# Optimization experiments

Hardware: AMD Instinct MI355X
Metric: run time of the kernel (lower is better)

Reference implementation:

```python
import jax, jax.numpy as jnp
import numpy as np

B, S, E, H, NQ, FF = 2, 2048, 768, 12, 8, 3072
DK = E // H
EPS = 1e-5


def _layernorm(x, g, b):
    m = jnp.mean(x, axis=-1, keepdims=True)
    v = jnp.mean((x - m) ** 2, axis=-1, keepdims=True)
    return (x - m) * jax.lax.rsqrt(v + EPS) * g + b


def setup_inputs() -> dict:
    key = jax.random.key(0)
    ks = jax.random.split(key, 12)
    s = 0.02
    return {
        'x': jax.random.normal(ks[0], (B, S, E), dtype=jnp.float32),
        'W_o': jax.random.normal(ks[1], (E, E), dtype=jnp.float32) * s,
        'b_o': jnp.zeros((E,), dtype=jnp.float32),
        'g1': jnp.ones((E,), dtype=jnp.float32),
        'be1': jnp.zeros((E,), dtype=jnp.float32),
        'g2': jnp.ones((E,), dtype=jnp.float32),
        'be2': jnp.zeros((E,), dtype=jnp.float32),
        'ry': jax.random.normal(ks[2], (NQ,), dtype=jnp.float32),
        'W1': jax.random.normal(ks[3], (NQ, FF), dtype=jnp.float32) * s,
        'b1': jnp.zeros((FF,), dtype=jnp.float32),
        'W2': jax.random.normal(ks[4], (FF, E), dtype=jnp.float32) * s,
        'b2': jnp.zeros((E,), dtype=jnp.float32),
    }


def reference(x, W_o, b_o, g1, be1, g2, be2, ry, W1, b1, W2, b2):
    # --- multi-head self-attention (q = k = v = x, no QKV projection) ---
    q = x.reshape(B, S, H, DK).transpose(0, 2, 1, 3)  # [B,H,S,DK]
    scores = jnp.einsum('bhqd,bhkd->bhqk', q, q) / jnp.sqrt(jnp.float32(DK))
    attn = jax.nn.softmax(scores, axis=-1)
    out = jnp.einsum('bhqk,bhkd->bhqd', attn, q)
    out = out.transpose(0, 2, 1, 3).reshape(B, S, E)
    attn_out = out @ W_o + b_o

    x = _layernorm(x + attn_out, g1, be1)

    # --- quantum FFN: per-wire RX(x_i) encode, RY(ry_i), <Z> = cos(x_i)*cos(ry_i) ---
    q_meas = jnp.cos(x[..., :NQ]) * jnp.cos(ry)  # [B,S,NQ]
    ffn_out = jax.nn.relu(q_meas @ W1 + b1) @ W2 + b2

    return _layernorm(x + ffn_out, g2, be2)
```

## Files before the change

kernel.cpp:

```cpp
#include <hip/hip_runtime.h>
#include <hip/hip_bf16.h>

#define B_  2
#define S_  2048
#define E_  768
#define H_  12
#define DK_ 64
#define NQ_ 8
#define FF_ 3072
#define EPS_ 1e-5f

typedef __attribute__((ext_vector_type(8))) short short8;
typedef __attribute__((ext_vector_type(4))) float f32x4;
typedef __hip_bfloat16 bf16;

__device__ __forceinline__ bf16 f2bh(float f) { return __float2bfloat16(f); }
__device__ __forceinline__ short f2b(float f) {
    bf16 h = __float2bfloat16(f);
    return *reinterpret_cast<short*>(&h);
}

__device__ __forceinline__ int swz(int row, int col) {
    return (col & 7) | ((((col >> 3) ^ (row & 7)) & 7) << 3);
}

__device__ __forceinline__ f32x4 mfma16(short8 a, short8 b, f32x4 c) {
    return __builtin_amdgcn_mfma_f32_16x16x32_bf16(a, b, c, 0, 0, 0);
}

__global__ __launch_bounds__(256) void prep_cvt(const float* __restrict__ x,
                                                bf16* __restrict__ xb, int n4) {
    int i = blockIdx.x * 256 + threadIdx.x;
    if (i >= n4) return;
    float4 f = *(const float4*)(x + (size_t)i * 4);
    short4 sv;
    sv.x = f2b(f.x); sv.y = f2b(f.y); sv.z = f2b(f.z); sv.w = f2b(f.w);
    *(short4*)((short*)xb + (size_t)i * 4) = sv;
}

__global__ __launch_bounds__(256) void transpose_cvt(const float* __restrict__ W,
                                                     bf16* __restrict__ WT,
                                                     int K, int N) {
    __shared__ float tile[32][33];
    int k0 = blockIdx.y * 32, n0 = blockIdx.x * 32;
    int tx = threadIdx.x & 31, ty = threadIdx.x >> 5;
#pragma unroll
    for (int i = 0; i < 4; i++) {
        int row = ty + i * 8;
        tile[row][tx] = W[(size_t)(k0 + row) * N + n0 + tx];
    }
    __syncthreads();
#pragma unroll
    for (int i = 0; i < 4; i++) {
        int row = ty + i * 8;
        WT[(size_t)(n0 + row) * K + k0 + tx] = f2bh(tile[tx][row]);
    }
}

__global__ __launch_bounds__(256) void attn_kernel(const bf16* __restrict__ xb,
                                                   bf16* __restrict__ out) {
    const int qtiles = S_ / 64;
    const int nwg = B_ * H_ * qtiles;
    int o = blockIdx.x;
    int blk = (o & 7) * (nwg >> 3) + (o >> 3);
    int qt = blk % qtiles;
    int hh = (blk / qtiles) % H_;
    int bb = blk / (qtiles * H_);
    const bf16* base = xb + (size_t)bb * S_ * E_ + hh * DK_;

    __shared__ __align__(16) bf16 Ks[64][64];
    __shared__ __align__(16) bf16 Vt[64][64];
    __shared__ __align__(16) bf16 Pl[4][16][64];

    int t = threadIdx.x;
    int w = t >> 6, l = t & 63, c = l & 15, g = l >> 4;

    short8 qf[2];
    {
        const bf16* qp = base + (size_t)(qt * 64 + w * 16 + c) * E_;
        qf[0] = *(const short8*)(qp + g * 8);
        qf[1] = *(const short8*)(qp + 32 + g * 8);
    }

    f32x4 oacc[4];
    float l_part[4];
#pragma unroll
    for (int n = 0; n < 4; n++) { oacc[n] = (f32x4){0.f, 0.f, 0.f, 0.f}; l_part[n] = 0.f; }

    int skey = t & 63;
    int scb0 = t >> 6;

    short8 pre[2];
#pragma unroll
    for (int it = 0; it < 2; it++)
        pre[it] = *(const short8*)(base + (size_t)skey * E_ + (scb0 + it * 4) * 8);

    for (int kt = 0; kt < S_ / 64; kt++) {
#pragma unroll
        for (int it = 0; it < 2; it++) {
            int cb = scb0 + it * 4;
            *(short8*)&Ks[skey][swz(skey, cb * 8)] = pre[it];
#pragma unroll
            for (int j = 0; j < 8; j++) {
                int d = cb * 8 + j;
                short sv = pre[it][j];
                Vt[d][swz(d, skey)] = *reinterpret_cast<bf16*>(&sv);
            }
        }
        __syncthreads();

        if (kt + 1 < S_ / 64) {
#pragma unroll
            for (int it = 0; it < 2; it++)
                pre[it] = *(const short8*)(base + (size_t)((kt + 1) * 64 + skey) * E_ + (scb0 + it * 4) * 8);
        }

        f32x4 sfr[4];
#pragma unroll
        for (int n = 0; n < 4; n++) {
            sfr[n] = (f32x4){0.f, 0.f, 0.f, 0.f};
#pragma unroll
            for (int kh = 0; kh < 2; kh++) {
                const short8 bfr = *(const short8*)&Ks[n * 16 + c][swz(n * 16 + c, kh * 32 + g * 8)];
                sfr[n] = mfma16(qf[kh], bfr, sfr[n]);
            }
        }
#pragma unroll
        for (int jj = 0; jj < 4; jj++) {
            float pv[4];
#pragma unroll
            for (int n = 0; n < 4; n++)
                pv[n] = exp2f(sfr[n][jj] * 0.18033688f);
            l_part[jj] += (pv[0] + pv[1]) + (pv[2] + pv[3]);
            int r = g * 4 + jj;
#pragma unroll
            for (int n = 0; n < 4; n++)
                Pl[w][r][swz(r, n * 16 + c)] = f2bh(pv[n]);
        }

#pragma unroll
        for (int ks = 0; ks < 2; ks++) {
            short8 vb[4];
#pragma unroll
            for (int dn = 0; dn < 4; dn++)
                vb[dn] = *(const short8*)&Vt[dn * 16 + c][swz(dn * 16 + c, ks * 32 + g * 8)];
            const short8 pa = *(const short8*)&Pl[w][c][swz(c, ks * 32 + g * 8)];
#pragma unroll
            for (int dn = 0; dn < 4; dn++)
                oacc[dn] = mfma16(pa, vb[dn], oacc[dn]);
        }
        __syncthreads();
    }

#pragma unroll
    for (int jj = 0; jj < 4; jj++) {
        float lv = l_part[jj];
#pragma unroll
        for (int msk = 1; msk < 16; msk <<= 1) lv += __shfl_xor(lv, msk);
        float inv = 1.f / lv;
        size_t ro = ((size_t)bb * S_ + qt * 64 + w * 16 + g * 4 + jj) * E_ + hh * DK_;
#pragma unroll
        for (int dn = 0; dn < 4; dn++)
            out[ro + dn * 16 + c] = f2bh(oacc[dn][jj] * inv);
    }
}

__global__ __launch_bounds__(256) void gemm_bf16(const bf16* __restrict__ A,
                                                 const bf16* __restrict__ BT,
                                                 const float* __restrict__ bias,
                                                 bf16* __restrict__ C,
                                                 int M, int N, int K) {
    __shared__ __align__(16) bf16 As[64][64];
    __shared__ __align__(16) bf16 Bs[64][64];
    int nbx = gridDim.x, nwg = nbx * gridDim.y;
    int id = blockIdx.y * nbx + blockIdx.x;
    int id2 = (nwg & 7) ? id : ((id & 7) * (nwg >> 3) + (id >> 3));
    int row0 = (id2 / nbx) * 64, col0 = (id2 % nbx) * 64;
    int t = threadIdx.x, w = t >> 6, l = t & 63, c = l & 15, g = l >> 4;

    f32x4 acc[4];
#pragma unroll
    for (int n = 0; n < 4; n++) acc[n] = (f32x4){0.f, 0.f, 0.f, 0.f};

    int srow = t & 63, scb = t >> 6;
    const bf16* arow_p = A + (size_t)(row0 + srow) * K;
    const bf16* brow_p = BT + (size_t)(col0 + srow) * K;

    short8 preA[2], preB[2];
#pragma unroll
    for (int it = 0; it < 2; it++) {
        preA[it] = *(const short8*)(arow_p + (scb + it * 4) * 8);
        preB[it] = *(const short8*)(brow_p + (scb + it * 4) * 8);
    }

    for (int k0 = 0; k0 < K; k0 += 64) {
#pragma unroll
        for (int it = 0; it < 2; it++) {
            int cb = scb + it * 4;
            *(short8*)&As[srow][swz(srow, cb * 8)] = preA[it];
            *(short8*)&Bs[srow][swz(srow, cb * 8)] = preB[it];
        }
        __syncthreads();
        if (k0 + 64 < K) {
#pragma unroll
            for (int it = 0; it < 2; it++) {
                preA[it] = *(const short8*)(arow_p + k0 + 64 + (scb + it * 4) * 8);
                preB[it] = *(const short8*)(brow_p + k0 + 64 + (scb + it * 4) * 8);
            }
        }
#pragma unroll
        for (int kh = 0; kh < 2; kh++) {
            const short8 af = *(const short8*)&As[w * 16 + c][swz(w * 16 + c, kh * 32 + g * 8)];
#pragma unroll
            for (int n = 0; n < 4; n++) {
                const short8 bfr = *(const short8*)&Bs[n * 16 + c][swz(n * 16 + c, kh * 32 + g * 8)];
                acc[n] = mfma16(af, bfr, acc[n]);
            }
        }
        __syncthreads();
    }
#pragma unroll
    for (int jj = 0; jj < 4; jj++) {
        int row = row0 + w * 16 + g * 4 + jj;
#pragma unroll
        for (int n = 0; n < 4; n++) {
            int col = col0 + n * 16 + c;
            C[(size_t)row * N + col] = f2bh(acc[n][jj] + bias[col]);
        }
    }
}

__global__ __launch_bounds__(256) void gemm2_mfma(const float* __restrict__ xln,
                                                  const float* __restrict__ ry,
                                                  const float* __restrict__ W1,
                                                  const float* __restrict__ b1,
                                                  const bf16* __restrict__ W2bT,
                                                  const float* __restrict__ b2,
                                                  bf16* __restrict__ C) {
    __shared__ __align__(16) bf16 As[64][64];
    __shared__ __align__(16) bf16 Bs[64][64];
    __shared__ __align__(16) bf16 W1t[64][8];
    __shared__ __align__(16) bf16 qm_s[64][8];
    const int nbx = E_ / 64;
    const int nwg = nbx * (B_ * S_ / 64);
    int id = blockIdx.y * nbx + blockIdx.x;
    int id2 = (id & 7) * (nwg >> 3) + (id >> 3);
    int row0 = (id2 / nbx) * 64, col0 = (id2 % nbx) * 64;
    int t = threadIdx.x, w = t >> 6, l = t & 63, c = l & 15, g = l >> 4;

    if (t < 64) {
        const float* xp = xln + (size_t)(row0 + t) * E_;
#pragma unroll
        for (int i = 0; i < NQ_; i++)
            qm_s[t][i] = f2bh(cosf(xp[i]) * cosf(ry[i]));
    }

    f32x4 acc[4];
#pragma unroll
    for (int n = 0; n < 4; n++) acc[n] = (f32x4){0.f, 0.f, 0.f, 0.f};

    int srow = t & 63, scb = t >> 6;
    int cl = t & 63, ib = t >> 6;
    const bf16* brow_p = W2bT + (size_t)(col0 + srow) * FF_;

    short8 preB[2];
    float preW1[2];
    float pb1[4];
#pragma unroll
    for (int it = 0; it < 2; it++)
        preB[it] = *(const short8*)(brow_p + (scb + it * 4) * 8);
    preW1[0] = W1[(size_t)ib * FF_ + cl];
    preW1[1] = W1[(size_t)(ib + 4) * FF_ + cl];
#pragma unroll
    for (int n = 0; n < 4; n++) pb1[n] = b1[n * 16 + c];

    __syncthreads();

    for (int k0 = 0; k0 < FF_; k0 += 64) {
        float b1c[4];
#pragma unroll
        for (int n = 0; n < 4; n++) b1c[n] = pb1[n];

#pragma unroll
        for (int it = 0; it < 2; it++)
            *(short8*)&Bs[srow][swz(srow, (scb + it * 4) * 8)] = preB[it];
        W1t[cl][ib]     = f2bh(preW1[0]);
        W1t[cl][ib + 4] = f2bh(preW1[1]);
        __syncthreads();

        if (k0 + 64 < FF_) {
#pragma unroll
            for (int it = 0; it < 2; it++)
                preB[it] = *(const short8*)(brow_p + k0 + 64 + (scb + it * 4) * 8);
            preW1[0] = W1[(size_t)ib * FF_ + k0 + 64 + cl];
            preW1[1] = W1[(size_t)(ib + 4) * FF_ + k0 + 64 + cl];
#pragma unroll
            for (int n = 0; n < 4; n++) pb1[n] = b1[k0 + 64 + n * 16 + c];
        }

        short8 zz = {0, 0, 0, 0, 0, 0, 0, 0};
        short8 aq = zz;
        if (g == 0) aq = *(const short8*)&qm_s[w * 16 + c][0];
        f32x4 zero4 = {0.f, 0.f, 0.f, 0.f};
#pragma unroll
        for (int n = 0; n < 4; n++) {
            short8 bw = zz;
            if (g == 0) bw = *(const short8*)&W1t[n * 16 + c][0];
            f32x4 hfr = mfma16(aq, bw, zero4);
#pragma unroll
            for (int jj = 0; jj < 4; jj++) {
                float hv = fmaxf(hfr[jj] + b1c[n], 0.f);
                int r = w * 16 + g * 4 + jj;
                As[r][swz(r, n * 16 + c)] = f2bh(hv);
            }
        }

#pragma unroll
        for (int kh = 0; kh < 2; kh++) {
            const short8 af = *(const short8*)&As[w * 16 + c][swz(w * 16 + c, kh * 32 + g * 8)];
#pragma unroll
            for (int n = 0; n < 4; n++) {
                const short8 bfr = *(const short8*)&Bs[n * 16 + c][swz(n * 16 + c, kh * 32 + g * 8)];
                acc[n] = mfma16(af, bfr, acc[n]);
            }
        }
        __syncthreads();
    }
#pragma unroll
    for (int jj = 0; jj < 4; jj++) {
        int row = row0 + w * 16 + g * 4 + jj;
#pragma unroll
        for (int n = 0; n < 4; n++) {
            int col = col0 + n * 16 + c;
            C[(size_t)row * E_ + col] = f2bh(acc[n][jj] + b2[col]);
        }
    }
}

__global__ __launch_bounds__(256) void gemm2_fused(const float* __restrict__ xln,
                                                   const float* __restrict__ ry,
                                                   const float* __restrict__ W1,
                                                   const float* __restrict__ b1,
                                                   const float* __restrict__ W2,
                                                   const float* __restrict__ b2,
                                                   bf16* __restrict__ C) {
    __shared__ __align__(16) bf16 As[64][64];
    __shared__ __align__(16) bf16 Bst[64][64];
    __shared__ float qmS[64][NQ_];
    int row0 = blockIdx.y * 64, col0 = blockIdx.x * 64;
    int t = threadIdx.x, w = t >> 6, l = t & 63, c = l & 15, g = l >> 4;

    for (int idx = t; idx < 64 * NQ_; idx += 256) {
        int r = idx >> 3, i = idx & 7;
        qmS[r][i] = cosf(xln[(size_t)(row0 + r) * E_ + i]) * cosf(ry[i]);
    }

    f32x4 acc[4];
#pragma unroll
    for (int n = 0; n < 4; n++) acc[n] = (f32x4){0.f, 0.f, 0.f, 0.f};

    int kl = t & 63, rg = (t >> 6) * 16;
    int brow = t >> 4, bcol = (t & 15) * 4;

    for (int k0 = 0; k0 < FF_; k0 += 64) {
        __syncthreads();
        {
            float w1v[NQ_];
#pragma unroll
            for (int i = 0; i < NQ_; i++) w1v[i] = W1[i * FF_ + k0 + kl];
            float b1v = b1[k0 + kl];
#pragma unroll
            for (int r16 = 0; r16 < 16; r16++) {
                int r = rg + r16;
                float sh = b1v;
#pragma unroll
                for (int i = 0; i < NQ_; i++) sh += qmS[r][i] * w1v[i];
                As[r][swz(r, kl)] = f2bh(fmaxf(sh, 0.f));
            }
        }
#pragma unroll
        for (int it = 0; it < 4; it++) {
            int kk = brow + it * 16;
            float4 v = *(const float4*)(W2 + (size_t)(k0 + kk) * E_ + col0 + bcol);
            Bst[bcol + 0][swz(bcol + 0, kk)] = f2bh(v.x);
            Bst[bcol + 1][swz(bcol + 1, kk)] = f2bh(v.y);
            Bst[bcol + 2][swz(bcol + 2, kk)] = f2bh(v.z);
            Bst[bcol + 3][swz(bcol + 3, kk)] = f2bh(v.w);
        }
        __syncthreads();
#pragma unroll
        for (int kh = 0; kh < 2; kh++) {
            const short8 af = *(const short8*)&As[w * 16 + c][swz(w * 16 + c, kh * 32 + g * 8)];
#pragma unroll
            for (int n = 0; n < 4; n++) {
                const short8 bfr = *(const short8*)&Bst[n * 16 + c][swz(n * 16 + c, kh * 32 + g * 8)];
                acc[n] = mfma16(af, bfr, acc[n]);
            }
        }
    }
#pragma unroll
    for (int jj = 0; jj < 4; jj++) {
        int row = row0 + w * 16 + g * 4 + jj;
#pragma unroll
        for (int n = 0; n < 4; n++) {
            int col = col0 + n * 16 + c;
            C[(size_t)row * E_ + col] = f2bh(acc[n][jj] + b2[col]);
        }
    }
}

__global__ __launch_bounds__(256) void ln_add_b(const float* __restrict__ X,
                                                const bf16* __restrict__ Yb,
                                                const float* __restrict__ g,
                                                const float* __restrict__ be,
                                                float* __restrict__ out) {
    int r = blockIdx.x;
    const size_t off = (size_t)r * E_;
    int t = threadIdx.x;
    float v[3];
    float s = 0.f, s2 = 0.f;
#pragma unroll
    for (int j = 0; j < 3; j++) {
        int e = t + j * 256;
        float val = X[off + e] + __bfloat162float(Yb[off + e]);
        v[j] = val; s += val; s2 += val * val;
    }
#pragma unroll
    for (int msk = 32; msk > 0; msk >>= 1) {
        s += __shfl_xor(s, msk);
        s2 += __shfl_xor(s2, msk);
    }
    __shared__ float red[8];
    int lane = t & 63, wv = t >> 6;
    if (lane == 0) { red[wv] = s; red[4 + wv] = s2; }
    __syncthreads();
    if (t == 0) {
        red[0] = red[0] + red[1] + red[2] + red[3];
        red[4] = red[4] + red[5] + red[6] + red[7];
    }
    __syncthreads();
    float mean = red[0] * (1.f / E_);
    float var = red[4] * (1.f / E_) - mean * mean;
    float inv = rsqrtf(var + EPS_);
#pragma unroll
    for (int j = 0; j < 3; j++) {
        int e = t + j * 256;
        out[off + e] = (v[j] - mean) * inv * g[e] + be[e];
    }
}

extern "C" void kernel_launch(void* const* d_in, const int* in_sizes, int n_in,
                              void* d_out, int out_size, void* d_ws, size_t ws_size,
                              hipStream_t stream) {
    const float* x   = (const float*)d_in[0];
    const float* W_o = (const float*)d_in[1];
    const float* b_o = (const float*)d_in[2];
    const float* g1  = (const float*)d_in[3];
    const float* be1 = (const float*)d_in[4];
    const float* g2  = (const float*)d_in[5];
    const float* be2 = (const float*)d_in[6];
    const float* ry  = (const float*)d_in[7];
    const float* W1  = (const float*)d_in[8];
    const float* b1  = (const float*)d_in[9];
    const float* W2  = (const float*)d_in[10];
    const float* b2  = (const float*)d_in[11];
    float* out = (float*)d_out;

    const size_t BSE = (size_t)B_ * S_ * E_;
    char* ws = (char*)d_ws;

    const size_t FAST_NEED = 37355520;
    bool fast = ws_size >= FAST_NEED;

    bf16* xb    = (bf16*)(ws + 0);
    bf16* attnb = (bf16*)(ws + 6291456);
    bf16* WobT  = fast ? (bf16*)(ws + 12582912) : (bf16*)(ws + 18874368);
    bf16* W2bT  = (bf16*)(ws + 13762560);
    bf16* tmp1b = fast ? (bf16*)(ws + 18481152) : (bf16*)(ws + 12582912);
    float* xln  = (float*)(ws + (fast ? 24772608 : 20054016));
    bf16* tmp2b = tmp1b;

    prep_cvt<<<dim3((BSE / 4 + 255) / 256), 256, 0, stream>>>(x, xb, BSE / 4);
    transpose_cvt<<<dim3(E_ / 32, E_ / 32), 256, 0, stream>>>(W_o, WobT, E_, E_);
    if (fast)
        transpose_cvt<<<dim3(E_ / 32, FF_ / 32), 256, 0, stream>>>(W2, W2bT, FF_, E_);

    attn_kernel<<<dim3(B_ * H_ * (S_ / 64)), 256, 0, stream>>>(xb, attnb);
    gemm_bf16<<<dim3(E_ / 64, (B_ * S_) / 64), 256, 0, stream>>>(
        attnb, WobT, b_o, tmp1b, B_ * S_, E_, E_);
    ln_add_b<<<dim3(B_ * S_), 256, 0, stream>>>(x, tmp1b, g1, be1, xln);

    if (fast) {
        gemm2_mfma<<<dim3(E_ / 64, (B_ * S_) / 64), 256, 0, stream>>>(
            xln, ry, W1, b1, W2bT, b2, tmp2b);
    } else {
        gemm2_fused<<<dim3(E_ / 64, (B_ * S_) / 64), 256, 0, stream>>>(
            xln, ry, W1, b1, W2, b2, tmp2b);
    }
    ln_add_b<<<dim3(B_ * S_), 256, 0, stream>>>(xln, tmp2b, g2, be2, out);
}
```

Before: 184.5 us.

## Double-buffer LDS tiles in both GEMMs and pre-transpose W1 to bf16

Both the output-projection GEMM and the fused quantum-FFN GEMM now keep two LDS stages. The next tile is written into the alternate buffer while the current one feeds the MFMAs, which removes one of the two barriers per K-step. A small new kernel converts W1 once to a bf16 [FF][NQ] layout, so each FFN block loads one 16-byte vector per row instead of gathering strided floats and converting them in the loop. The cost is double the LDS for the B tiles, which may lower occupancy, plus a larger workspace requirement for the fast path.

```diff
diff --git a/kernel.cpp b/kernel.cpp
--- a/kernel.cpp
+++ b/kernel.cpp
@@ -55,6 +55,16 @@
         int row = ty + i * 8;
         WT[(size_t)(n0 + row) * K + k0 + tx] = f2bh(tile[tx][row]);
     }
+}
+
+__global__ __launch_bounds__(256) void prep_w1t(const float* __restrict__ W1,
+                                                bf16* __restrict__ W1bT) {
+    int k = blockIdx.x * 256 + threadIdx.x;
+    if (k >= FF_) return;
+    short8 v;
+#pragma unroll
+    for (int i = 0; i < NQ_; i++) v[i] = f2b(W1[(size_t)i * FF_ + k]);
+    *(short8*)(W1bT + (size_t)k * NQ_) = v;
 }
 
 __global__ __launch_bounds__(256) void attn_kernel(const bf16* __restrict__ xb,
@@ -170,8 +180,8 @@
                                                  const float* __restrict__ bias,
                                                  bf16* __restrict__ C,
                                                  int M, int N, int K) {
-    __shared__ __align__(16) bf16 As[64][64];
-    __shared__ __align__(16) bf16 Bs[64][64];
+    __shared__ __align__(16) bf16 As2[2][64][64];
+    __shared__ __align__(16) bf16 Bs2[2][64][64];
     int nbx = gridDim.x, nwg = nbx * gridDim.y;
     int id = blockIdx.y * nbx + blockIdx.x;
     int id2 = (nwg & 7) ? id : ((id & 7) * (nwg >> 3) + (id >> 3));
@@ -183,37 +193,47 @@
     for (int n = 0; n < 4; n++) acc[n] = (f32x4){0.f, 0.f, 0.f, 0.f};
 
     int srow = t & 63, scb = t >> 6;
-    const bf16* arow_p = A + (size_t)(row0 + srow) * K;
-    const bf16* brow_p = BT + (size_t)(col0 + srow) * K;
-
-    short8 preA[2], preB[2];
-#pragma unroll
-    for (int it = 0; it < 2; it++) {
-        preA[it] = *(const short8*)(arow_p + (scb + it * 4) * 8);
-        preB[it] = *(const short8*)(brow_p + (scb + it * 4) * 8);
-    }
-
-    for (int k0 = 0; k0 < K; k0 += 64) {
-#pragma unroll
-        for (int it = 0; it < 2; it++) {
-            int cb = scb + it * 4;
-            *(short8*)&As[srow][swz(srow, cb * 8)] = preA[it];
-            *(short8*)&Bs[srow][swz(srow, cb * 8)] = preB[it];
-        }
-        __syncthreads();
+    const bf16* ap = A + (size_t)(row0 + srow) * K;
+    const bf16* bp = BT + (size_t)(col0 + srow) * K;
+
+    short8 pA0, pA1, pB0, pB1;
+    pA0 = *(const short8*)(ap + scb * 8);
+    pA1 = *(const short8*)(ap + (scb + 4) * 8);
+    pB0 = *(const short8*)(bp + scb * 8);
+    pB1 = *(const short8*)(bp + (scb + 4) * 8);
+    *(short8*)&As2[0][srow][swz(srow, scb * 8)] = pA0;
+    *(short8*)&As2[0][srow][swz(srow, (scb + 4) * 8)] = pA1;
+    *(short8*)&Bs2[0][srow][swz(srow, scb * 8)] = pB0;
+    *(short8*)&Bs2[0][srow][swz(srow, (scb + 4) * 8)] = pB1;
+    if (64 < K) {
+        pA0 = *(const short8*)(ap + 64 + scb * 8);
+        pA1 = *(const short8*)(ap + 64 + (scb + 4) * 8);
+        pB0 = *(const short8*)(bp + 64 + scb * 8);
+        pB1 = *(const short8*)(bp + 64 + (scb + 4) * 8);
+    }
+    __syncthreads();
+
+    int cur = 0;
+    for (int k0 = 0; k0 < K; k0 += 64, cur ^= 1) {
+        int nxt = cur ^ 1;
         if (k0 + 64 < K) {
-#pragma unroll
-            for (int it = 0; it < 2; it++) {
-                preA[it] = *(const short8*)(arow_p + k0 + 64 + (scb + it * 4) * 8);
-                preB[it] = *(const short8*)(brow_p + k0 + 64 + (scb + it * 4) * 8);
-            }
+            *(short8*)&As2[nxt][srow][swz(srow, scb * 8)] = pA0;
+            *(short8*)&As2[nxt][srow][swz(srow, (scb + 4) * 8)] = pA1;
+            *(short8*)&Bs2[nxt][srow][swz(srow, scb * 8)] = pB0;
+            *(short8*)&Bs2[nxt][srow][swz(srow, (scb + 4) * 8)] = pB1;
+        }
+        if (k0 + 128 < K) {
+            pA0 = *(const short8*)(ap + k0 + 128 + scb * 8);
+            pA1 = *(const short8*)(ap + k0 + 128 + (scb + 4) * 8);
+            pB0 = *(const short8*)(bp + k0 + 128 + scb * 8);
+            pB1 = *(const short8*)(bp + k0 + 128 + (scb + 4) * 8);
         }
 #pragma unroll
         for (int kh = 0; kh < 2; kh++) {
-            const short8 af = *(const short8*)&As[w * 16 + c][swz(w * 16 + c, kh * 32 + g * 8)];
+            const short8 af = *(const short8*)&As2[cur][w * 16 + c][swz(w * 16 + c, kh * 32 + g * 8)];
 #pragma unroll
             for (int n = 0; n < 4; n++) {
-                const short8 bfr = *(const short8*)&Bs[n * 16 + c][swz(n * 16 + c, kh * 32 + g * 8)];
+                const short8 bfr = *(const short8*)&Bs2[cur][n * 16 + c][swz(n * 16 + c, kh * 32 + g * 8)];
                 acc[n] = mfma16(af, bfr, acc[n]);
             }
         }
@@ -232,14 +252,14 @@
 
 __global__ __launch_bounds__(256) void gemm2_mfma(const float* __restrict__ xln,
                                                   const float* __restrict__ ry,
-                                                  const float* __restrict__ W1,
+                                                  const bf16* __restrict__ W1bT,
                                                   const float* __restrict__ b1,
                                                   const bf16* __restrict__ W2bT,
                                                   const float* __restrict__ b2,
                                                   bf16* __restrict__ C) {
     __shared__ __align__(16) bf16 As[64][64];
-    __shared__ __align__(16) bf16 Bs[64][64];
-    __shared__ __align__(16) bf16 W1t[64][8];
+    __shared__ __align__(16) bf16 Bs[2][64][64];
+    __shared__ __align__(16) bf16 W1t[2][64][8];
     __shared__ __align__(16) bf16 qm_s[64][8];
     const int nbx = E_ / 64;
     const int nwg = nbx * (B_ * S_ / 64);
@@ -260,52 +280,47 @@
     for (int n = 0; n < 4; n++) acc[n] = (f32x4){0.f, 0.f, 0.f, 0.f};
 
     int srow = t & 63, scb = t >> 6;
-    int cl = t & 63, ib = t >> 6;
     const bf16* brow_p = W2bT + (size_t)(col0 + srow) * FF_;
 
-    short8 preB[2];
-    float preW1[2];
-    float pb1[4];
-#pragma unroll
-    for (int it = 0; it < 2; it++)
-        preB[it] = *(const short8*)(brow_p + (scb + it * 4) * 8);
-    preW1[0] = W1[(size_t)ib * FF_ + cl];
-    preW1[1] = W1[(size_t)(ib + 4) * FF_ + cl];
-#pragma unroll
-    for (int n = 0; n < 4; n++) pb1[n] = b1[n * 16 + c];
-
+    short8 preB0, preB1, preW;
+    preB0 = *(const short8*)(brow_p + scb * 8);
+    preB1 = *(const short8*)(brow_p + (scb + 4) * 8);
+    if (t < 64) preW = *(const short8*)(W1bT + (size_t)t * NQ_);
+    *(short8*)&Bs[0][srow][swz(srow, scb * 8)] = preB0;
+    *(short8*)&Bs[0][srow][swz(srow, (scb + 4) * 8)] = preB1;
+    if (t < 64) *(short8*)&W1t[0][t][0] = preW;
+    preB0 = *(const short8*)(brow_p + 64 + scb * 8);
+    preB1 = *(const short8*)(brow_p + 64 + (scb + 4) * 8);
+    if (t < 64) preW = *(const short8*)(W1bT + (size_t)(64 + t) * NQ_);
     __syncthreads();
 
-    for (int k0 = 0; k0 < FF_; k0 += 64) {
+    short8 zz = {0, 0, 0, 0, 0, 0, 0, 0};
+    short8 aq = zz;
+    if (g == 0) aq = *(const short8*)&qm_s[w * 16 + c][0];
+
+    int cur = 0;
+    for (int k0 = 0; k0 < FF_; k0 += 64, cur ^= 1) {
         float b1c[4];
 #pragma unroll
-        for (int n = 0; n < 4; n++) b1c[n] = pb1[n];
-
-#pragma unroll
-        for (int it = 0; it < 2; it++)
-            *(short8*)&Bs[srow][swz(srow, (scb + it * 4) * 8)] = preB[it];
-        W1t[cl][ib]     = f2bh(preW1[0]);
-        W1t[cl][ib + 4] = f2bh(preW1[1]);
-        __syncthreads();
-
+        for (int n = 0; n < 4; n++) b1c[n] = b1[k0 + n * 16 + c];
+
+        int nxt = cur ^ 1;
         if (k0 + 64 < FF_) {
-#pragma unroll
-            for (int it = 0; it < 2; it++)
-                preB[it] = *(const short8*)(brow_p + k0 + 64 + (scb + it * 4) * 8);
-            preW1[0] = W1[(size_t)ib * FF_ + k0 + 64 + cl];
-            preW1[1] = W1[(size_t)(ib + 4) * FF_ + k0 + 64 + cl];
-#pragma unroll
-            for (int n = 0; n < 4; n++) pb1[n] = b1[k0 + 64 + n * 16 + c];
-        }
-
-        short8 zz = {0, 0, 0, 0, 0, 0, 0, 0};
-        short8 aq = zz;
-        if (g == 0) aq = *(const short8*)&qm_s[w * 16 + c][0];
+            *(short8*)&Bs[nxt][srow][swz(srow, scb * 8)] = preB0;
+            *(short8*)&Bs[nxt][srow][swz(srow, (scb + 4) * 8)] = preB1;
+            if (t < 64) *(short8*)&W1t[nxt][t][0] = preW;
+        }
+        if (k0 + 128 < FF_) {
+            preB0 = *(const short8*)(brow_p + k0 + 128 + scb * 8);
+            preB1 = *(const short8*)(brow_p + k0 + 128 + (scb + 4) * 8);
+            if (t < 64) preW = *(const short8*)(W1bT + (size_t)(k0 + 128 + t) * NQ_);
+        }
+
         f32x4 zero4 = {0.f, 0.f, 0.f, 0.f};
 #pragma unroll
         for (int n = 0; n < 4; n++) {
             short8 bw = zz;
-            if (g == 0) bw = *(const short8*)&W1t[n * 16 + c][0];
+            if (g == 0) bw = *(const short8*)&W1t[cur][n * 16 + c][0];
             f32x4 hfr = mfma16(aq, bw, zero4);
 #pragma unroll
             for (int jj = 0; jj < 4; jj++) {
@@ -320,7 +335,7 @@
             const short8 af = *(const short8*)&As[w * 16 + c][swz(w * 16 + c, kh * 32 + g * 8)];
 #pragma unroll
             for (int n = 0; n < 4; n++) {
-                const short8 bfr = *(const short8*)&Bs[n * 16 + c][swz(n * 16 + c, kh * 32 + g * 8)];
+                const short8 bfr = *(const short8*)&Bs[cur][n * 16 + c][swz(n * 16 + c, kh * 32 + g * 8)];
                 acc[n] = mfma16(af, bfr, acc[n]);
             }
         }
@@ -469,7 +484,7 @@
     const size_t BSE = (size_t)B_ * S_ * E_;
     char* ws = (char*)d_ws;
 
-    const size_t FAST_NEED = 37355520;
+    const size_t FAST_NEED = 37404672;
     bool fast = ws_size >= FAST_NEED;
 
     bf16* xb    = (bf16*)(ws + 0);
@@ -478,12 +493,15 @@
     bf16* W2bT  = (bf16*)(ws + 13762560);
     bf16* tmp1b = fast ? (bf16*)(ws + 18481152) : (bf16*)(ws + 12582912);
     float* xln  = (float*)(ws + (fast ? 24772608 : 20054016));
+    bf16* W1bT  = (bf16*)(ws + 37355520);
     bf16* tmp2b = tmp1b;
 
     prep_cvt<<<dim3((BSE / 4 + 255) / 256), 256, 0, stream>>>(x, xb, BSE / 4);
     transpose_cvt<<<dim3(E_ / 32, E_ / 32), 256, 0, stream>>>(W_o, WobT, E_, E_);
-    if (fast)
+    if (fast) {
         transpose_cvt<<<dim3(E_ / 32, FF_ / 32), 256, 0, stream>>>(W2, W2bT, FF_, E_);
+        prep_w1t<<<dim3(FF_ / 256), 256, 0, stream>>>(W1, W1bT);
+    }
 
     attn_kernel<<<dim3(B_ * H_ * (S_ / 64)), 256, 0, stream>>>(xb, attnb);
     gemm_bf16<<<dim3(E_ / 64, (B_ * S_) / 64), 256, 0, stream>>>(
@@ -492,7 +510,7 @@
 
     if (fast) {
         gemm2_mfma<<<dim3(E_ / 64, (B_ * S_) / 64), 256, 0, stream>>>(
-            xln, ry, W1, b1, W2bT, b2, tmp2b);
+            xln, ry, W1bT, b1, W2bT, b2, tmp2b);
     } else {
         gemm2_fused<<<dim3(E_ / 64, (B_ * S_) / 64), 256, 0, stream>>>(
             xln, ry, W1, b1, W2, b2, tmp2b);
```

Measured after the change: 178.7 us. 3.1% less time.
